# Performance work log

Hardware: AMD Instinct MI355X
Metric: run time of the kernel (lower is better)

## Reference

```python
import jax, jax.numpy as jnp
import numpy as np

N = 50000      # nodes
E = 800000     # random edges (self-loops appended, per PyG add_self_loops=True)
IN = 256       # input_dim
HID = 64       # hidden_dim (per-head out_channels)
H = 4          # heads (hardcoded in GAT)
OUT = 64       # output_dim
NEG_SLOPE = 0.2  # PyG GATv2Conv default negative_slope


def setup_inputs() -> dict:
    key = jax.random.key(0)
    ks = jax.random.split(key, 24)
    g = lambda i, shape: jax.random.normal(ks[i], shape, jnp.float32) * 0.05
    inp = {
        "x": jax.random.normal(ks[0], (N, IN), jnp.float32),
        "edge_index": jax.random.randint(ks[1], (2, E), 0, N, dtype=jnp.int32),
        # conv1: GATv2Conv(IN, HID, heads=4)
        "W1l": g(2, (IN, H * HID)), "b1l": g(3, (H * HID,)),
        "W1r": g(4, (IN, H * HID)), "b1r": g(5, (H * HID,)),
        "att1": g(6, (H, HID)), "bias1": g(7, (H * HID,)),
        # conv2: GATv2Conv(4*HID, HID, heads=4)
        "W2l": g(8, (H * HID, H * HID)), "b2l": g(9, (H * HID,)),
        "W2r": g(10, (H * HID, H * HID)), "b2r": g(11, (H * HID,)),
        "att2": g(12, (H, HID)), "bias2": g(13, (H * HID,)),
        # post_mp: Linear(4*HID, HID) -> Dropout -> Linear(HID, OUT)
        "Wp1": g(14, (H * HID, HID)), "bp1": g(15, (HID,)),
        "Wp2": g(16, (HID, OUT)), "bp2": g(17, (OUT,)),
    }
    return inp


def _gatv2_layer(x, src, dst, Wl, bl, Wr, br, att, bias):
    # GATv2Conv (concat=True): x_l = lin_l(x) for sources, x_r = lin_r(x) for targets
    C = att.shape[1]
    xl = (x @ Wl + bl).reshape(-1, H, C)   # [N,H,C]
    xr = (x @ Wr + br).reshape(-1, H, C)
    e = jax.nn.leaky_relu(xl[src] + xr[dst], NEG_SLOPE)     # [E',H,C]
    logits = jnp.einsum('ehc,hc->eh', e, att)               # [E',H]
    # segment softmax over destination nodes (self-loops guarantee nonempty segments)
    m = jax.ops.segment_max(logits, dst, num_segments=N)
    p = jnp.exp(logits - m[dst])
    s = jax.ops.segment_sum(p, dst, num_segments=N)
    alpha = p / s[dst]                                      # [E',H]
    out = jax.ops.segment_sum(xl[src] * alpha[..., None], dst, num_segments=N)
    return out.reshape(-1, H * C) + bias                    # [N,H*C]


def reference(x, edge_index, W1l, b1l, W1r, b1r, att1, bias1,
              W2l, b2l, W2r, b2r, att2, bias2, Wp1, bp1, Wp2, bp2):
    # add self-loops (PyG GATv2Conv default add_self_loops=True)
    loops = jnp.arange(N, dtype=edge_index.dtype)
    src = jnp.concatenate([edge_index[0], loops])
    dst = jnp.concatenate([edge_index[1], loops])
    h = _gatv2_layer(x, src, dst, W1l, b1l, W1r, b1r, att1, bias1)
    h = jax.nn.relu(h)  # dropout p=0.6 is identity in eval mode
    h = _gatv2_layer(h, src, dst, W2l, b2l, W2r, b2r, att2, bias2)
    h = jax.nn.relu(h)
    h = h @ Wp1 + bp1   # post_mp (dropout identity in eval)
    h = h @ Wp2 + bp2
    return h
```

## Files before the change

kernel.cpp:

```cpp
#include <hip/hip_runtime.h>

typedef unsigned short u16;
typedef short bf16x8 __attribute__((ext_vector_type(8)));
typedef float f32x4 __attribute__((ext_vector_type(4)));

__device__ __forceinline__ u16 f2bf(float f) {
    unsigned u = __float_as_uint(f);
    return (u16)((u + 0x7fffu + ((u >> 16) & 1u)) >> 16);
}
__device__ __forceinline__ float exp2_hw(float x) {
    float r;
    asm("v_exp_f32 %0, %1" : "=v"(r) : "v"(x));
    return r;
}
template <int CTRL>
__device__ __forceinline__ float dpp_add(float p) {
    int t = __builtin_amdgcn_update_dpp(0, __float_as_int(p), CTRL, 0xf, 0xf, true);
    return p + __int_as_float(t);
}
__device__ __forceinline__ void gload_lds16(const u16* g, u16* lds) {
    __builtin_amdgcn_global_load_lds((const __attribute__((address_space(1))) void*)g,
                                     (__attribute__((address_space(3))) void*)lds, 16, 0, 0);
}

struct MegaP {
    const float* x; const int* ei;
    const float *W1l, *b1l, *W1r, *b1r, *att1, *bias1;
    const float *W2l, *b2l, *W2r, *b2r, *att2, *bias2;
    const float *Wp1, *bp1, *Wp2, *bp2;
    u16 *Abuf, *XLR, *WB1, *WB2, *Wpt;
    float *bc1, *bc2, *bpf;
    int *cnt; u16 *slot;
    float* outF;
    int N, E, Mpad, Mt;
};


template <bool AF32, int BN, bool F32OUT>
__device__ __forceinline__ void gemm_tile(const void* __restrict__ Av, const u16* __restrict__ Bt,
                                          const float* __restrict__ bias, void* __restrict__ out,
                                          int M, int Nout, int bm, int bn, u16* As, u16* Bs) {
    constexpr int K = 256;
    constexpr int NRF = BN / 64;
    const int tid = threadIdx.x;
    const int l = tid & 63;
    const int w = tid >> 6;
    const int wm = w >> 2, wn = w & 3;
    const int lrow = l & 15, lk = l >> 4;
    const int wbase = tid & ~63;

#pragma unroll
    for (int it = 0; it < BN / 16; ++it) {
        int c = it * 512 + tid;
        int col = c >> 5, kc = c & 31;
        bf16x8 v = *(const bf16x8*)(Bt + (size_t)(bn * BN + col) * K + kc * 8);
        *(bf16x8*)(Bs + col * K + ((kc ^ (col & 7)) * 8)) = v;
    }

    auto stageA = [&](int ks) {
        if (AF32) {
            const float* A32 = (const float*)Av;
#pragma unroll
            for (int it = 0; it < 2; ++it) {
                int c = it * 512 + tid;
                int row = c >> 3, seg = c & 7;
                int grow = bm * 128 + row;
                if (grow > M - 1) grow = M - 1;
                const float* sp = A32 + (size_t)grow * K + ks * 64 + seg * 8;
                float4 v0 = *(const float4*)sp;
                float4 v1 = *(const float4*)(sp + 4);
                bf16x8 pk;
                pk[0] = (short)f2bf(v0.x); pk[1] = (short)f2bf(v0.y);
                pk[2] = (short)f2bf(v0.z); pk[3] = (short)f2bf(v0.w);
                pk[4] = (short)f2bf(v1.x); pk[5] = (short)f2bf(v1.y);
                pk[6] = (short)f2bf(v1.z); pk[7] = (short)f2bf(v1.w);
                *(bf16x8*)(As + row * 64 + ((seg ^ (row & 7)) * 8)) = pk;
            }
        } else {
            const u16* Abf = (const u16*)Av;
#pragma unroll
            for (int it = 0; it < 2; ++it) {
                int c = it * 512 + tid;
                int row = c >> 3, seg = c & 7;
                int ssrc = seg ^ (row & 7);
                gload_lds16(Abf + (size_t)(bm * 128 + row) * K + ks * 64 + ssrc * 8,
                            As + (size_t)(it * 512 + wbase) * 8);
            }
        }
    };

    f32x4 acc[4][NRF];
#pragma unroll
    for (int m = 0; m < 4; ++m)
#pragma unroll
        for (int n = 0; n < NRF; ++n) acc[m][n] = (f32x4){0.f, 0.f, 0.f, 0.f};

    stageA(0);
    __syncthreads();

    for (int ks = 0; ks < 4; ++ks) {
#pragma unroll
        for (int h = 0; h < 2; ++h) {
            bf16x8 av[4], bv[NRF];
#pragma unroll
            for (int m = 0; m < 4; ++m) {
                int row = wm * 64 + m * 16 + lrow;
                int seg = ((h * 4 + lk) ^ (row & 7));
                av[m] = *(const bf16x8*)(As + row * 64 + seg * 8);
            }
#pragma unroll
            for (int n = 0; n < NRF; ++n) {
                int col = wn * (NRF * 16) + n * 16 + lrow;
                int kc = ks * 8 + h * 4 + lk;
                bv[n] = *(const bf16x8*)(Bs + col * K + ((kc ^ (col & 7)) * 8));
            }
#pragma unroll
            for (int m = 0; m < 4; ++m)
#pragma unroll
                for (int n = 0; n < NRF; ++n)
                    acc[m][n] = __builtin_amdgcn_mfma_f32_16x16x32_bf16(av[m], bv[n], acc[m][n], 0, 0, 0);
        }
        if (ks < 3) {
            __syncthreads();
            stageA(ks + 1);
            __syncthreads();
        }
    }

    float bl[NRF];
#pragma unroll
    for (int n = 0; n < NRF; ++n) bl[n] = bias[bn * BN + wn * (NRF * 16) + n * 16 + lrow];

#pragma unroll
    for (int m = 0; m < 4; ++m) {
        int grow = bm * 128 + wm * 64 + m * 16 + lk * 4;
#pragma unroll
        for (int j = 0; j < 4; ++j) {
            if (grow + j < M) {
#pragma unroll
                for (int n = 0; n < NRF; ++n) {
                    int col = bn * BN + wn * (NRF * 16) + n * 16 + lrow;
                    float v = acc[m][n][j] + bl[n];
                    if (F32OUT)
                        ((float*)out)[(size_t)(grow + j) * Nout + col] = v;
                    else
                        ((u16*)out)[(size_t)(grow + j) * Nout + col] = f2bf(v);
                }
            }
        }
    }
}

__device__ __forceinline__ void tile_map4(int d, int Mt, int& bm, int& bn) {
    int nfull = (Mt & ~7) * 4;
    if (d < nfull) {
        int g = d >> 5, r = d & 31;
        bm = g * 8 + (r & 7);
        bn = r >> 3;
    } else {
        int idx = d - nfull;
        bm = (Mt & ~7) + (idx >> 2);
        bn = idx & 3;
    }
}


__global__ __launch_bounds__(256) void k_prep(MegaP P) {
    const int N = P.N, E = P.E;
    const int c0 = 1024, c1 = c0 + 64, c2 = c1 + 4;
    int b = blockIdx.x;
    int tid = threadIdx.x;
    if (b < c0) {
        int n = b & 255, m = b >> 8;
        const float* W = (m == 0) ? P.W1l : (m == 1) ? P.W1r : (m == 2) ? P.W2l : P.W2r;
        u16* dst = (m < 2) ? P.WB1 : P.WB2;
        dst[(size_t)((m & 1) * 256 + n) * 256 + tid] = f2bf(W[(size_t)tid * 256 + n]);
    } else if (b < c1) {
        int j = b - c0;
        float a = 0.f;
        for (int k = 0; k < 64; ++k) a += P.Wp1[tid * 64 + k] * P.Wp2[k * 64 + j];
        P.Wpt[j * 256 + tid] = f2bf(a);
        if (tid == 0) {
            float bb = P.bp2[j];
            for (int k = 0; k < 64; ++k) bb += P.bp1[k] * P.Wp2[k * 64 + j];
            P.bpf[j] = bb;
        }
    } else if (b < c2) {
        int m = b - c1;
        const float* s = (m == 0) ? P.b1l : (m == 1) ? P.b1r : (m == 2) ? P.b2l : P.b2r;
        float* d = (m < 2) ? P.bc1 : P.bc2;
        d[(m & 1) * 256 + tid] = s[tid];
    } else {
        int bi = b - c2;
        int xcd = bi & 7;
        int e = (bi >> 3) * 256 + tid;
        if (e < E) {
            int dst = P.ei[E + e];
            int S = (N + 7) >> 3;
            if ((unsigned)(dst - xcd * S) < (unsigned)S) {
                int src = P.ei[e];
                int p = atomicAdd(P.cnt + dst, 1);
                if (p < 64) P.slot[((size_t)dst << 6) + p] = (u16)src;
            }
        }
    }
}


__global__ __launch_bounds__(512) void k_g1(MegaP P) {
    __shared__ __align__(16) u16 As[8192];
    __shared__ __align__(16) u16 Bs[32768];
    int bm, bn;
    tile_map4(blockIdx.x, P.Mt, bm, bn);
    gemm_tile<true, 128, false>(P.x, P.WB1, P.bc1, P.XLR, P.N, 512, bm, bn, As, Bs);
}

__global__ __launch_bounds__(512) void k_g2(MegaP P) {
    __shared__ __align__(16) u16 As[8192];
    __shared__ __align__(16) u16 Bs[32768];
    int bm, bn;
    tile_map4(blockIdx.x, P.Mt, bm, bn);
    gemm_tile<false, 128, false>(P.Abuf, P.WB2, P.bc2, P.XLR, P.N, 512, bm, bn, As, Bs);
}

__global__ __launch_bounds__(512) void k_gp(MegaP P) {
    __shared__ __align__(16) u16 As[8192];
    __shared__ __align__(16) u16 Bs[16384];
    gemm_tile<false, 64, true>(P.Abuf, P.Wpt, P.bpf, P.outF, P.N, 64, blockIdx.x, 0, As, Bs);
}


__global__ __launch_bounds__(256) void k_edge(const int* __restrict__ cnt,
                                              const u16* __restrict__ slot,
                                              const u16* __restrict__ XLR,
                                              const float* __restrict__ att,
                                              const float* __restrict__ bias,
                                              u16* __restrict__ H, int N) {
    int wid0 = blockIdx.x * 4 + (threadIdx.x >> 6);
    if (wid0 >= N) return;
    const int wid = __builtin_amdgcn_readfirstlane(wid0);
    const int l = threadIdx.x & 63;

    const float LOG2E = 1.4426950408889634f;
    float4 a4 = *(const float4*)(att + l * 4);
    a4.x *= LOG2E; a4.y *= LOG2E; a4.z *= LOG2E; a4.w *= LOG2E;
    float4 bb = *(const float4*)(bias + l * 4);
    const char* Xb = (const char*)XLR;
    const int lofs = l << 3;

    uint2 xr = *(const uint2*)(Xb + ((size_t)wid << 10) + 512 + lofs);
    float r0 = __uint_as_float(xr.x << 16), r1 = __uint_as_float(xr.x & 0xffff0000u);
    float r2 = __uint_as_float(xr.y << 16), r3 = __uint_as_float(xr.y & 0xffff0000u);

    const u16* sl = slot + ((size_t)wid << 6);
    int deg = cnt[wid];
    if (deg > 64) deg = 64;
    float s = 0.f, o0 = 0.f, o1 = 0.f, o2 = 0.f, o3 = 0.f;

    auto edge1 = [&](uint2 wv) {
        float c0 = __uint_as_float(wv.x << 16), c1 = __uint_as_float(wv.x & 0xffff0000u);
        float c2 = __uint_as_float(wv.y << 16), c3 = __uint_as_float(wv.y & 0xffff0000u);
        float t0 = c0 + r0, t1 = c1 + r1, t2 = c2 + r2, t3 = c3 + r3;
        t0 = fmaf(-0.8f, fminf(t0, 0.f), t0);
        t1 = fmaf(-0.8f, fminf(t1, 0.f), t1);
        t2 = fmaf(-0.8f, fminf(t2, 0.f), t2);
        t3 = fmaf(-0.8f, fminf(t3, 0.f), t3);
        float p = t0 * a4.x; p = fmaf(t1, a4.y, p); p = fmaf(t2, a4.z, p); p = fmaf(t3, a4.w, p);
        p = dpp_add<0xB1>(p);
        p = dpp_add<0x4E>(p);
        p = dpp_add<0x141>(p);
        p = dpp_add<0x140>(p);
        float e = exp2_hw(p);
        s += e;
        o0 = fmaf(e, c0, o0); o1 = fmaf(e, c1, o1);
        o2 = fmaf(e, c2, o2); o3 = fmaf(e, c3, o3);
    };

    {
        uint2 w0 = *(const uint2*)(Xb + ((size_t)wid << 10) + lofs);
        edge1(w0);
    }

    int i = 0;
    for (; i + 8 <= deg; i += 8) {
        int u0 = __builtin_amdgcn_readfirstlane(sl[i]);
        int u1 = __builtin_amdgcn_readfirstlane(sl[i + 1]);
        int u2 = __builtin_amdgcn_readfirstlane(sl[i + 2]);
        int u3 = __builtin_amdgcn_readfirstlane(sl[i + 3]);
        int u4 = __builtin_amdgcn_readfirstlane(sl[i + 4]);
        int u5 = __builtin_amdgcn_readfirstlane(sl[i + 5]);
        int u6 = __builtin_amdgcn_readfirstlane(sl[i + 6]);
        int u7 = __builtin_amdgcn_readfirstlane(sl[i + 7]);
        uint2 w0 = *(const uint2*)(Xb + ((size_t)u0 << 10) + lofs);
        uint2 w1 = *(const uint2*)(Xb + ((size_t)u1 << 10) + lofs);
        uint2 w2 = *(const uint2*)(Xb + ((size_t)u2 << 10) + lofs);
        uint2 w3 = *(const uint2*)(Xb + ((size_t)u3 << 10) + lofs);
        uint2 w4 = *(const uint2*)(Xb + ((size_t)u4 << 10) + lofs);
        uint2 w5 = *(const uint2*)(Xb + ((size_t)u5 << 10) + lofs);
        uint2 w6 = *(const uint2*)(Xb + ((size_t)u6 << 10) + lofs);
        uint2 w7 = *(const uint2*)(Xb + ((size_t)u7 << 10) + lofs);
        edge1(w0); edge1(w1); edge1(w2); edge1(w3);
        edge1(w4); edge1(w5); edge1(w6); edge1(w7);
    }
    for (; i + 4 <= deg; i += 4) {
        int u0 = __builtin_amdgcn_readfirstlane(sl[i]);
        int u1 = __builtin_amdgcn_readfirstlane(sl[i + 1]);
        int u2 = __builtin_amdgcn_readfirstlane(sl[i + 2]);
        int u3 = __builtin_amdgcn_readfirstlane(sl[i + 3]);
        uint2 w0 = *(const uint2*)(Xb + ((size_t)u0 << 10) + lofs);
        uint2 w1 = *(const uint2*)(Xb + ((size_t)u1 << 10) + lofs);
        uint2 w2 = *(const uint2*)(Xb + ((size_t)u2 << 10) + lofs);
        uint2 w3 = *(const uint2*)(Xb + ((size_t)u3 << 10) + lofs);
        edge1(w0); edge1(w1); edge1(w2); edge1(w3);
    }
    for (; i < deg; ++i) {
        int u0 = __builtin_amdgcn_readfirstlane(sl[i]);
        uint2 w0 = *(const uint2*)(Xb + ((size_t)u0 << 10) + lofs);
        edge1(w0);
    }

    float inv = 1.f / s;
    o0 = fmaxf(fmaf(o0, inv, bb.x), 0.f);
    o1 = fmaxf(fmaf(o1, inv, bb.y), 0.f);
    o2 = fmaxf(fmaf(o2, inv, bb.z), 0.f);
    o3 = fmaxf(fmaf(o3, inv, bb.w), 0.f);
    ushort4 w4 = {f2bf(o0), f2bf(o1), f2bf(o2), f2bf(o3)};
    *(ushort4*)(H + ((size_t)wid << 8) + l * 4) = w4;
}


extern "C" void kernel_launch(void* const* d_in, const int* in_sizes, int n_in,
                              void* d_out, int out_size, void* d_ws, size_t ws_size,
                              hipStream_t stream) {
    MegaP P;
    P.x     = (const float*)d_in[0];
    P.ei    = (const int*)d_in[1];
    P.W1l   = (const float*)d_in[2];  P.b1l  = (const float*)d_in[3];
    P.W1r   = (const float*)d_in[4];  P.b1r  = (const float*)d_in[5];
    P.att1  = (const float*)d_in[6];  P.bias1 = (const float*)d_in[7];
    P.W2l   = (const float*)d_in[8];  P.b2l  = (const float*)d_in[9];
    P.W2r   = (const float*)d_in[10]; P.b2r  = (const float*)d_in[11];
    P.att2  = (const float*)d_in[12]; P.bias2 = (const float*)d_in[13];
    P.Wp1   = (const float*)d_in[14]; P.bp1  = (const float*)d_in[15];
    P.Wp2   = (const float*)d_in[16]; P.bp2  = (const float*)d_in[17];

    const int N = in_sizes[0] / 256;
    const int E = in_sizes[1] / 2;
    const int Mpad = ((N + 127) / 128) * 128;

    char* ws = (char*)d_ws;
    size_t o = 0;
    auto alloc = [&](size_t b) { char* p = ws + o; o = (o + b + 255) & ~(size_t)255; return p; };
    P.Abuf   = (u16*)alloc((size_t)Mpad * 256 * 2);
    P.XLR    = (u16*)alloc((size_t)Mpad * 512 * 2);
    P.WB1    = (u16*)alloc(512 * 256 * 2);
    P.WB2    = (u16*)alloc(512 * 256 * 2);
    P.Wpt    = (u16*)alloc(64 * 256 * 2);
    P.bc1    = (float*)alloc(512 * 4);
    P.bc2    = (float*)alloc(512 * 4);
    P.bpf    = (float*)alloc(64 * 4);
    P.cnt    = (int*)alloc((size_t)N * 4);
    P.slot   = (u16*)alloc((size_t)N * 64 * 2);
    P.outF   = (float*)d_out;
    P.N = N; P.E = E; P.Mpad = Mpad; P.Mt = Mpad / 128;

    hipMemsetAsync(P.cnt, 0, (size_t)N * 4, stream);
    if (Mpad > N)
        hipMemsetAsync(P.Abuf + (size_t)N * 256, 0, (size_t)(Mpad - N) * 256 * 2, stream);

    const int nScat = ((E + 255) / 256) * 8;
    k_prep<<<1024 + 64 + 4 + nScat, 256, 0, stream>>>(P);

    const int ntile = P.Mt * 4;
    const int egrid = (N + 3) / 4;
    k_g1<<<ntile, 512, 0, stream>>>(P);
    k_edge<<<egrid, 256, 0, stream>>>(P.cnt, P.slot, P.XLR, P.att1, P.bias1, P.Abuf, N);
    k_g2<<<ntile, 512, 0, stream>>>(P);
    k_edge<<<egrid, 256, 0, stream>>>(P.cnt, P.slot, P.XLR, P.att2, P.bias2, P.Abuf, N);
    k_gp<<<P.Mt, 512, 0, stream>>>(P);
}
```

Measured before the change: 249.9 us.

## Restructure GEMMs to stage full A row-panel once and stream B fragments from global

Each GEMM block now loads its entire 128x256 A tile into LDS once and loops over all output column panels. The per-tile B staging into LDS is replaced by direct global reads from a weight buffer that the prep kernel pre-permutes into MFMA fragment order. This removes the redundant A reloads across four column tiles and the repeated B staging and syncs. In exchange the grid is 4x smaller (fewer blocks, 64KB LDS each) and every B operand read now goes to global/L2 instead of LDS.

```diff
diff --git a/kernel.cpp b/kernel.cpp
--- a/kernel.cpp
+++ b/kernel.cpp
@@ -28,7 +28,7 @@
     const float *W1l, *b1l, *W1r, *b1r, *att1, *bias1;
     const float *W2l, *b2l, *W2r, *b2r, *att2, *bias2;
     const float *Wp1, *bp1, *Wp2, *bp2;
-    u16 *Abuf, *XLR, *WB1, *WB2, *Wpt;
+    u16 *Abuf, *XLR, *BF1, *BF2, *BFp;
     float *bc1, *bc2, *bpf;
     int *cnt; u16 *slot;
     float* outF;
@@ -36,12 +36,12 @@
 };
 
 
-template <bool AF32, int BN, bool F32OUT>
-__device__ __forceinline__ void gemm_tile(const void* __restrict__ Av, const u16* __restrict__ Bt,
-                                          const float* __restrict__ bias, void* __restrict__ out,
-                                          int M, int Nout, int bm, int bn, u16* As, u16* Bs) {
+template <bool AF32, int NRF, int CT, bool F32OUT>
+__device__ __forceinline__ void gemm_v2(const void* __restrict__ Av, const u16* __restrict__ Bf,
+                                        const float* __restrict__ bias, void* __restrict__ out,
+                                        int M, int Nout, int bm, u16* As) {
     constexpr int K = 256;
-    constexpr int NRF = BN / 64;
+    constexpr int PANEL = NRF * 64;
     const int tid = threadIdx.x;
     const int l = tid & 63;
     const int w = tid >> 6;
@@ -49,70 +49,58 @@
     const int lrow = l & 15, lk = l >> 4;
     const int wbase = tid & ~63;
 
-#pragma unroll
-    for (int it = 0; it < BN / 16; ++it) {
-        int c = it * 512 + tid;
-        int col = c >> 5, kc = c & 31;
-        bf16x8 v = *(const bf16x8*)(Bt + (size_t)(bn * BN + col) * K + kc * 8);
-        *(bf16x8*)(Bs + col * K + ((kc ^ (col & 7)) * 8)) = v;
-    }
-
-    auto stageA = [&](int ks) {
-        if (AF32) {
-            const float* A32 = (const float*)Av;
-#pragma unroll
-            for (int it = 0; it < 2; ++it) {
-                int c = it * 512 + tid;
-                int row = c >> 3, seg = c & 7;
-                int grow = bm * 128 + row;
-                if (grow > M - 1) grow = M - 1;
-                const float* sp = A32 + (size_t)grow * K + ks * 64 + seg * 8;
-                float4 v0 = *(const float4*)sp;
-                float4 v1 = *(const float4*)(sp + 4);
-                bf16x8 pk;
-                pk[0] = (short)f2bf(v0.x); pk[1] = (short)f2bf(v0.y);
-                pk[2] = (short)f2bf(v0.z); pk[3] = (short)f2bf(v0.w);
-                pk[4] = (short)f2bf(v1.x); pk[5] = (short)f2bf(v1.y);
-                pk[6] = (short)f2bf(v1.z); pk[7] = (short)f2bf(v1.w);
-                *(bf16x8*)(As + row * 64 + ((seg ^ (row & 7)) * 8)) = pk;
-            }
-        } else {
-            const u16* Abf = (const u16*)Av;
-#pragma unroll
-            for (int it = 0; it < 2; ++it) {
-                int c = it * 512 + tid;
-                int row = c >> 3, seg = c & 7;
-                int ssrc = seg ^ (row & 7);
-                gload_lds16(Abf + (size_t)(bm * 128 + row) * K + ks * 64 + ssrc * 8,
-                            As + (size_t)(it * 512 + wbase) * 8);
-            }
-        }
-    };
-
-    f32x4 acc[4][NRF];
-#pragma unroll
-    for (int m = 0; m < 4; ++m)
-#pragma unroll
-        for (int n = 0; n < NRF; ++n) acc[m][n] = (f32x4){0.f, 0.f, 0.f, 0.f};
-
-    stageA(0);
+    if (AF32) {
+        const float* A32 = (const float*)Av;
+#pragma unroll
+        for (int it = 0; it < 8; ++it) {
+            int c = it * 512 + tid;
+            int row = c >> 5, ch = c & 31;
+            int grow = bm * 128 + row;
+            if (grow > M - 1) grow = M - 1;
+            int ssrc = ch ^ (row & 7);
+            const float* sp = A32 + (size_t)grow * K + ssrc * 8;
+            float4 v0 = *(const float4*)sp;
+            float4 v1 = *(const float4*)(sp + 4);
+            bf16x8 pk;
+            pk[0] = (short)f2bf(v0.x); pk[1] = (short)f2bf(v0.y);
+            pk[2] = (short)f2bf(v0.z); pk[3] = (short)f2bf(v0.w);
+            pk[4] = (short)f2bf(v1.x); pk[5] = (short)f2bf(v1.y);
+            pk[6] = (short)f2bf(v1.z); pk[7] = (short)f2bf(v1.w);
+            *(bf16x8*)(As + (size_t)c * 8) = pk;
+        }
+    } else {
+        const u16* Abf = (const u16*)Av;
+#pragma unroll
+        for (int it = 0; it < 8; ++it) {
+            int c = it * 512 + tid;
+            int row = c >> 5, ch = c & 31;
+            int ssrc = ch ^ (row & 7);
+            gload_lds16(Abf + (size_t)(bm * 128 + row) * K + ssrc * 8,
+                        As + (size_t)(it * 512 + wbase) * 8);
+        }
+    }
     __syncthreads();
 
-    for (int ks = 0; ks < 4; ++ks) {
-#pragma unroll
-        for (int h = 0; h < 2; ++h) {
+    for (int bn = 0; bn < CT; ++bn) {
+        f32x4 acc[4][NRF];
+#pragma unroll
+        for (int m = 0; m < 4; ++m)
+#pragma unroll
+            for (int n = 0; n < NRF; ++n) acc[m][n] = (f32x4){0.f, 0.f, 0.f, 0.f};
+
+#pragma unroll
+        for (int ks = 0; ks < 8; ++ks) {
+            const int kc = ks * 4 + lk;
             bf16x8 av[4], bv[NRF];
 #pragma unroll
             for (int m = 0; m < 4; ++m) {
                 int row = wm * 64 + m * 16 + lrow;
-                int seg = ((h * 4 + lk) ^ (row & 7));
-                av[m] = *(const bf16x8*)(As + row * 64 + seg * 8);
+                av[m] = *(const bf16x8*)(As + row * K + ((kc ^ (row & 7)) * 8));
             }
 #pragma unroll
             for (int n = 0; n < NRF; ++n) {
-                int col = wn * (NRF * 16) + n * 16 + lrow;
-                int kc = ks * 8 + h * 4 + lk;
-                bv[n] = *(const bf16x8*)(Bs + col * K + ((kc ^ (col & 7)) * 8));
+                int g = bn * (4 * NRF) + wn * NRF + n;
+                bv[n] = *(const bf16x8*)(Bf + ((size_t)g * 32 + kc) * 128 + lrow * 8);
             }
 #pragma unroll
             for (int m = 0; m < 4; ++m)
@@ -120,47 +108,29 @@
                 for (int n = 0; n < NRF; ++n)
                     acc[m][n] = __builtin_amdgcn_mfma_f32_16x16x32_bf16(av[m], bv[n], acc[m][n], 0, 0, 0);
         }
-        if (ks < 3) {
-            __syncthreads();
-            stageA(ks + 1);
-            __syncthreads();
-        }
-    }
-
-    float bl[NRF];
-#pragma unroll
-    for (int n = 0; n < NRF; ++n) bl[n] = bias[bn * BN + wn * (NRF * 16) + n * 16 + lrow];
-
-#pragma unroll
-    for (int m = 0; m < 4; ++m) {
-        int grow = bm * 128 + wm * 64 + m * 16 + lk * 4;
-#pragma unroll
-        for (int j = 0; j < 4; ++j) {
-            if (grow + j < M) {
-#pragma unroll
-                for (int n = 0; n < NRF; ++n) {
-                    int col = bn * BN + wn * (NRF * 16) + n * 16 + lrow;
-                    float v = acc[m][n][j] + bl[n];
-                    if (F32OUT)
-                        ((float*)out)[(size_t)(grow + j) * Nout + col] = v;
-                    else
-                        ((u16*)out)[(size_t)(grow + j) * Nout + col] = f2bf(v);
+
+        float bl[NRF];
+#pragma unroll
+        for (int n = 0; n < NRF; ++n) bl[n] = bias[bn * PANEL + wn * (NRF * 16) + n * 16 + lrow];
+
+#pragma unroll
+        for (int m = 0; m < 4; ++m) {
+            int grow = bm * 128 + wm * 64 + m * 16 + lk * 4;
+#pragma unroll
+            for (int j = 0; j < 4; ++j) {
+                if (grow + j < M) {
+#pragma unroll
+                    for (int n = 0; n < NRF; ++n) {
+                        int col = bn * PANEL + wn * (NRF * 16) + n * 16 + lrow;
+                        float v = acc[m][n][j] + bl[n];
+                        if (F32OUT)
+                            ((float*)out)[(size_t)(grow + j) * Nout + col] = v;
+                        else
+                            ((u16*)out)[(size_t)(grow + j) * Nout + col] = f2bf(v);
+                    }
                 }
             }
         }
-    }
-}
-
-__device__ __forceinline__ void tile_map4(int d, int Mt, int& bm, int& bn) {
-    int nfull = (Mt & ~7) * 4;
-    if (d < nfull) {
-        int g = d >> 5, r = d & 31;
-        bm = g * 8 + (r & 7);
-        bn = r >> 3;
-    } else {
-        int idx = d - nfull;
-        bm = (Mt & ~7) + (idx >> 2);
-        bn = idx & 3;
     }
 }
 
@@ -173,13 +143,16 @@
     if (b < c0) {
         int n = b & 255, m = b >> 8;
         const float* W = (m == 0) ? P.W1l : (m == 1) ? P.W1r : (m == 2) ? P.W2l : P.W2r;
-        u16* dst = (m < 2) ? P.WB1 : P.WB2;
-        dst[(size_t)((m & 1) * 256 + n) * 256 + tid] = f2bf(W[(size_t)tid * 256 + n]);
+        u16* dst = (m < 2) ? P.BF1 : P.BF2;
+        int col = (m & 1) * 256 + n;
+        int k = tid;
+        dst[((size_t)(col >> 4) * 32 + (k >> 3)) * 128 + (col & 15) * 8 + (k & 7)] =
+            f2bf(W[(size_t)k * 256 + n]);
     } else if (b < c1) {
         int j = b - c0;
         float a = 0.f;
         for (int k = 0; k < 64; ++k) a += P.Wp1[tid * 64 + k] * P.Wp2[k * 64 + j];
-        P.Wpt[j * 256 + tid] = f2bf(a);
+        P.BFp[((size_t)(j >> 4) * 32 + (tid >> 3)) * 128 + (j & 15) * 8 + (tid & 7)] = f2bf(a);
         if (tid == 0) {
             float bb = P.bp2[j];
             for (int k = 0; k < 64; ++k) bb += P.bp1[k] * P.Wp2[k * 64 + j];
@@ -208,25 +181,16 @@
 
 
 __global__ __launch_bounds__(512) void k_g1(MegaP P) {
-    __shared__ __align__(16) u16 As[8192];
-    __shared__ __align__(16) u16 Bs[32768];
-    int bm, bn;
-    tile_map4(blockIdx.x, P.Mt, bm, bn);
-    gemm_tile<true, 128, false>(P.x, P.WB1, P.bc1, P.XLR, P.N, 512, bm, bn, As, Bs);
-}
-
+    __shared__ __align__(16) u16 As[32768];
+    gemm_v2<true, 2, 4, false>(P.x, P.BF1, P.bc1, P.XLR, P.N, 512, blockIdx.x, As);
+}
 __global__ __launch_bounds__(512) void k_g2(MegaP P) {
-    __shared__ __align__(16) u16 As[8192];
-    __shared__ __align__(16) u16 Bs[32768];
-    int bm, bn;
-    tile_map4(blockIdx.x, P.Mt, bm, bn);
-    gemm_tile<false, 128, false>(P.Abuf, P.WB2, P.bc2, P.XLR, P.N, 512, bm, bn, As, Bs);
-}
-
+    __shared__ __align__(16) u16 As[32768];
+    gemm_v2<false, 2, 4, false>(P.Abuf, P.BF2, P.bc2, P.XLR, P.N, 512, blockIdx.x, As);
+}
 __global__ __launch_bounds__(512) void k_gp(MegaP P) {
-    __shared__ __align__(16) u16 As[8192];
-    __shared__ __align__(16) u16 Bs[16384];
-    gemm_tile<false, 64, true>(P.Abuf, P.Wpt, P.bpf, P.outF, P.N, 64, blockIdx.x, 0, As, Bs);
+    __shared__ __align__(16) u16 As[32768];
+    gemm_v2<false, 1, 1, true>(P.Abuf, P.BFp, P.bpf, P.outF, P.N, 64, blockIdx.x, As);
 }
 
 
@@ -353,9 +317,9 @@
     auto alloc = [&](size_t b) { char* p = ws + o; o = (o + b + 255) & ~(size_t)255; return p; };
     P.Abuf   = (u16*)alloc((size_t)Mpad * 256 * 2);
     P.XLR    = (u16*)alloc((size_t)Mpad * 512 * 2);
-    P.WB1    = (u16*)alloc(512 * 256 * 2);
-    P.WB2    = (u16*)alloc(512 * 256 * 2);
-    P.Wpt    = (u16*)alloc(64 * 256 * 2);
+    P.BF1    = (u16*)alloc(512 * 256 * 2);
+    P.BF2    = (u16*)alloc(512 * 256 * 2);
+    P.BFp    = (u16*)alloc(64 * 256 * 2);
     P.bc1    = (float*)alloc(512 * 4);
     P.bc2    = (float*)alloc(512 * 4);
     P.bpf    = (float*)alloc(64 * 4);
@@ -371,11 +335,10 @@
     const int nScat = ((E + 255) / 256) * 8;
     k_prep<<<1024 + 64 + 4 + nScat, 256, 0, stream>>>(P);
 
-    const int ntile = P.Mt * 4;
     const int egrid = (N + 3) / 4;
-    k_g1<<<ntile, 512, 0, stream>>>(P);
+    k_g1<<<P.Mt, 512, 0, stream>>>(P);
     k_edge<<<egrid, 256, 0, stream>>>(P.cnt, P.slot, P.XLR, P.att1, P.bias1, P.Abuf, N);
-    k_g2<<<ntile, 512, 0, stream>>>(P);
+    k_g2<<<P.Mt, 512, 0, stream>>>(P);
     k_edge<<<egrid, 256, 0, stream>>>(P.cnt, P.slot, P.XLR, P.att2, P.bias2, P.Abuf, N);
     k_gp<<<P.Mt, 512, 0, stream>>>(P);
 }
```

Result: slower. 275.4 us (+10.2%).

## Overlap edge scatter with first GEMM and pack edge math into float2

Applied to the files above, without the earlier changes.

The edge-bucketing scatter moves out of the prep kernel and into extra blocks of the first GEMM launch, so the atomic scatter runs alongside the GEMM tiles instead of before them. Scatter blocks now cover 512 edges each. The per-edge attention math in k_edge is rewritten with float2 vectors so the compiler can emit packed FP32 ops, and leaky-relu becomes max(t, 0.2t). Scatter blocks share the GEMM kernel's large LDS allocation and 512-thread launch bounds, which may limit how many can be resident at once.

```diff
diff --git a/kernel.cpp b/kernel.cpp
--- a/kernel.cpp
+++ b/kernel.cpp
@@ -3,6 +3,7 @@
 typedef unsigned short u16;
 typedef short bf16x8 __attribute__((ext_vector_type(8)));
 typedef float f32x4 __attribute__((ext_vector_type(4)));
+typedef float f32x2 __attribute__((ext_vector_type(2)));
 
 __device__ __forceinline__ u16 f2bf(float f) {
     unsigned u = __float_as_uint(f);
@@ -166,8 +167,7 @@
 
 
 __global__ __launch_bounds__(256) void k_prep(MegaP P) {
-    const int N = P.N, E = P.E;
-    const int c0 = 1024, c1 = c0 + 64, c2 = c1 + 4;
+    const int c0 = 1024, c1 = c0 + 64;
     int b = blockIdx.x;
     int tid = threadIdx.x;
     if (b < c0) {
@@ -185,15 +185,27 @@
             for (int k = 0; k < 64; ++k) bb += P.bp1[k] * P.Wp2[k * 64 + j];
             P.bpf[j] = bb;
         }
-    } else if (b < c2) {
+    } else {
         int m = b - c1;
         const float* s = (m == 0) ? P.b1l : (m == 1) ? P.b1r : (m == 2) ? P.b2l : P.b2r;
         float* d = (m < 2) ? P.bc1 : P.bc2;
         d[(m & 1) * 256 + tid] = s[tid];
+    }
+}
+
+
+__global__ __launch_bounds__(512) void k_g1(MegaP P, int ntile) {
+    __shared__ __align__(16) u16 As[8192];
+    __shared__ __align__(16) u16 Bs[32768];
+    if ((int)blockIdx.x < ntile) {
+        int bm, bn;
+        tile_map4(blockIdx.x, P.Mt, bm, bn);
+        gemm_tile<true, 128, false>(P.x, P.WB1, P.bc1, P.XLR, P.N, 512, bm, bn, As, Bs);
     } else {
-        int bi = b - c2;
+        const int N = P.N, E = P.E;
+        int bi = (int)blockIdx.x - ntile;
         int xcd = bi & 7;
-        int e = (bi >> 3) * 256 + tid;
+        int e = (bi >> 3) * 512 + threadIdx.x;
         if (e < E) {
             int dst = P.ei[E + e];
             int S = (N + 7) >> 3;
@@ -204,15 +216,6 @@
             }
         }
     }
-}
-
-
-__global__ __launch_bounds__(512) void k_g1(MegaP P) {
-    __shared__ __align__(16) u16 As[8192];
-    __shared__ __align__(16) u16 Bs[32768];
-    int bm, bn;
-    tile_map4(blockIdx.x, P.Mt, bm, bn);
-    gemm_tile<true, 128, false>(P.x, P.WB1, P.bc1, P.XLR, P.N, 512, bm, bn, As, Bs);
 }
 
 __global__ __launch_bounds__(512) void k_g2(MegaP P) {
@@ -243,37 +246,41 @@
 
     const float LOG2E = 1.4426950408889634f;
     float4 a4 = *(const float4*)(att + l * 4);
-    a4.x *= LOG2E; a4.y *= LOG2E; a4.z *= LOG2E; a4.w *= LOG2E;
+    f32x2 aA = {a4.x * LOG2E, a4.y * LOG2E};
+    f32x2 aB = {a4.z * LOG2E, a4.w * LOG2E};
     float4 bb = *(const float4*)(bias + l * 4);
     const char* Xb = (const char*)XLR;
     const int lofs = l << 3;
 
     uint2 xr = *(const uint2*)(Xb + ((size_t)wid << 10) + 512 + lofs);
-    float r0 = __uint_as_float(xr.x << 16), r1 = __uint_as_float(xr.x & 0xffff0000u);
-    float r2 = __uint_as_float(xr.y << 16), r3 = __uint_as_float(xr.y & 0xffff0000u);
+    f32x2 rA = {__uint_as_float(xr.x << 16), __uint_as_float(xr.x & 0xffff0000u)};
+    f32x2 rB = {__uint_as_float(xr.y << 16), __uint_as_float(xr.y & 0xffff0000u)};
 
     const u16* sl = slot + ((size_t)wid << 6);
     int deg = cnt[wid];
     if (deg > 64) deg = 64;
-    float s = 0.f, o0 = 0.f, o1 = 0.f, o2 = 0.f, o3 = 0.f;
+    float s = 0.f;
+    f32x2 oA = {0.f, 0.f}, oB = {0.f, 0.f};
 
     auto edge1 = [&](uint2 wv) {
-        float c0 = __uint_as_float(wv.x << 16), c1 = __uint_as_float(wv.x & 0xffff0000u);
-        float c2 = __uint_as_float(wv.y << 16), c3 = __uint_as_float(wv.y & 0xffff0000u);
-        float t0 = c0 + r0, t1 = c1 + r1, t2 = c2 + r2, t3 = c3 + r3;
-        t0 = fmaf(-0.8f, fminf(t0, 0.f), t0);
-        t1 = fmaf(-0.8f, fminf(t1, 0.f), t1);
-        t2 = fmaf(-0.8f, fminf(t2, 0.f), t2);
-        t3 = fmaf(-0.8f, fminf(t3, 0.f), t3);
-        float p = t0 * a4.x; p = fmaf(t1, a4.y, p); p = fmaf(t2, a4.z, p); p = fmaf(t3, a4.w, p);
+        f32x2 cA = {__uint_as_float(wv.x << 16), __uint_as_float(wv.x & 0xffff0000u)};
+        f32x2 cB = {__uint_as_float(wv.y << 16), __uint_as_float(wv.y & 0xffff0000u)};
+        f32x2 tA = cA + rA, tB = cB + rB;
+        f32x2 uA = tA * 0.2f, uB = tB * 0.2f;
+        tA.x = fmaxf(tA.x, uA.x); tA.y = fmaxf(tA.y, uA.y);
+        tB.x = fmaxf(tB.x, uB.x); tB.y = fmaxf(tB.y, uB.y);
+        f32x2 pd = tA * aA;
+        pd = __builtin_elementwise_fma(tB, aB, pd);
+        float p = pd.x + pd.y;
         p = dpp_add<0xB1>(p);
         p = dpp_add<0x4E>(p);
         p = dpp_add<0x141>(p);
         p = dpp_add<0x140>(p);
         float e = exp2_hw(p);
         s += e;
-        o0 = fmaf(e, c0, o0); o1 = fmaf(e, c1, o1);
-        o2 = fmaf(e, c2, o2); o3 = fmaf(e, c3, o3);
+        f32x2 ee = {e, e};
+        oA = __builtin_elementwise_fma(ee, cA, oA);
+        oB = __builtin_elementwise_fma(ee, cB, oB);
     };
 
     {
@@ -320,10 +327,10 @@
     }
 
     float inv = 1.f / s;
-    o0 = fmaxf(fmaf(o0, inv, bb.x), 0.f);
-    o1 = fmaxf(fmaf(o1, inv, bb.y), 0.f);
-    o2 = fmaxf(fmaf(o2, inv, bb.z), 0.f);
-    o3 = fmaxf(fmaf(o3, inv, bb.w), 0.f);
+    float o0 = fmaxf(fmaf(oA.x, inv, bb.x), 0.f);
+    float o1 = fmaxf(fmaf(oA.y, inv, bb.y), 0.f);
+    float o2 = fmaxf(fmaf(oB.x, inv, bb.z), 0.f);
+    float o3 = fmaxf(fmaf(oB.y, inv, bb.w), 0.f);
     ushort4 w4 = {f2bf(o0), f2bf(o1), f2bf(o2), f2bf(o3)};
     *(ushort4*)(H + ((size_t)wid << 8) + l * 4) = w4;
 }
@@ -368,12 +375,13 @@
     if (Mpad > N)
         hipMemsetAsync(P.Abuf + (size_t)N * 256, 0, (size_t)(Mpad - N) * 256 * 2, stream);
 
-    const int nScat = ((E + 255) / 256) * 8;
-    k_prep<<<1024 + 64 + 4 + nScat, 256, 0, stream>>>(P);
+    k_prep<<<1024 + 64 + 4, 256, 0, stream>>>(P);
 
     const int ntile = P.Mt * 4;
+    const int nScat = ((E + 511) / 512) * 8;
+    k_g1<<<ntile + nScat, 512, 0, stream>>>(P, ntile);
+
     const int egrid = (N + 3) / 4;
-    k_g1<<<ntile, 512, 0, stream>>>(P);
     k_edge<<<egrid, 256, 0, stream>>>(P.cnt, P.slot, P.XLR, P.att1, P.bias1, P.Abuf, N);
     k_g2<<<ntile, 512, 0, stream>>>(P);
     k_edge<<<egrid, 256, 0, stream>>>(P.cnt, P.slot, P.XLR, P.att2, P.bias2, P.Abuf, N);
```

After: 247.8 us. About the same (-0.9%).
